# Performance work log

Measured on AMD Instinct MI355X. Metric: run time of the kernel, lower is better.

The kernel has to match this reference:

```python
import jax, jax.numpy as jnp
import numpy as np

IN_FEATURES = 1024
OUT_FEATURES = 1024
BATCH = 32768
EPS = 1e-6


def setup_inputs() -> dict:
    key = jax.random.key(0)
    kx, kw = jax.random.split(key)
    x = jax.random.normal(kx, (BATCH, IN_FEATURES), dtype=jnp.float32)
    # xavier-uniform-like init for weight [out, in]
    limit = np.sqrt(6.0 / (IN_FEATURES + OUT_FEATURES)).astype(np.float32)
    W = jax.random.uniform(kw, (OUT_FEATURES, IN_FEATURES), dtype=jnp.float32,
                           minval=-limit, maxval=limit)
    b = jnp.zeros((OUT_FEATURES,), dtype=jnp.float32)
    return {"x": x, "W": W, "b": b}


def reference(x, W, b):
    # sign with sign(0) -> +1
    binary_w = jnp.where(W >= 0, 1.0, -1.0).astype(W.dtype)  # [out, in]
    # per-output-row scale, detached in the original (no grad flows through it)
    scale = jnp.maximum(jnp.mean(jnp.abs(W), axis=1, keepdims=True), EPS)  # [out, 1]
    # F.linear(x, binary_w * scale, b) = x @ (binary_w * scale).T + b
    return jnp.einsum('ni,oi->no', x, binary_w * scale) + b
```

## Files before the change

### kernel.cpp

```cpp
#include <hip/hip_runtime.h>


typedef short short8 __attribute__((ext_vector_type(8)));
typedef float f32x4 __attribute__((ext_vector_type(4)));

#define BATCH 32768
#define IN_F  1024
#define OUT_F 1024
#define EPS   1e-6f

__device__ __forceinline__ ushort f2bf(float f) {
  unsigned u = __builtin_bit_cast(unsigned, f);
  u += 0x7FFFu + ((u >> 16) & 1u);
  return (ushort)(u >> 16);
}

__device__ __forceinline__ void gload_lds16(const void* g, void* l) {
  __builtin_amdgcn_global_load_lds(
      (const __attribute__((address_space(1))) unsigned*)g,
      (__attribute__((address_space(3))) unsigned*)l, 16, 0, 0);
}

__global__ void bin_kernel(const float* __restrict__ W,
                           ushort* __restrict__ Wb,
                           float* __restrict__ scale) {
  int row = blockIdx.x * 4 + (threadIdx.x >> 6);
  int t = threadIdx.x & 63;
  const float4* wr = (const float4*)(W + (size_t)row * IN_F);
  ushort4* wb = (ushort4*)(Wb + (size_t)row * IN_F);
  float s = 0.f;
#pragma unroll
  for (int i = 0; i < 4; ++i) {
    float4 v = wr[i * 64 + t];
    ushort4 u;
    u.x = (v.x >= 0.f) ? 0x3F80 : 0xBF80;
    u.y = (v.y >= 0.f) ? 0x3F80 : 0xBF80;
    u.z = (v.z >= 0.f) ? 0x3F80 : 0xBF80;
    u.w = (v.w >= 0.f) ? 0x3F80 : 0xBF80;
    wb[i * 64 + t] = u;
    s += fabsf(v.x) + fabsf(v.y) + fabsf(v.z) + fabsf(v.w);
  }
#pragma unroll
  for (int o = 32; o > 0; o >>= 1) s += __shfl_down(s, o);
  if (t == 0) scale[row] = fmaxf(s * (1.0f / (float)IN_F), EPS);
}

__global__ void cvt_kernel(const float* __restrict__ X,
                           ushort* __restrict__ Xb) {
  size_t idx = (size_t)blockIdx.x * 256 + threadIdx.x;
  float4 v = ((const float4*)X)[idx];
  ushort4 u;
  u.x = f2bf(v.x); u.y = f2bf(v.y); u.z = f2bf(v.z); u.w = f2bf(v.w);
  ((ushort4*)Xb)[idx] = u;
}

__device__ __forceinline__ void rd4(short8 (*dst)[2], const char* base,
                                    int c0, int c1) {
#pragma unroll
  for (int m = 0; m < 4; ++m) {
    dst[m][0] = *(const short8*)(base + m * 2048 + c0);
    dst[m][1] = *(const short8*)(base + m * 2048 + c1);
  }
}
__device__ __forceinline__ void rd2(short8 (*dst)[2], const char* base,
                                    int c0, int c1) {
#pragma unroll
  for (int n = 0; n < 2; ++n) {
    dst[n][0] = *(const short8*)(base + n * 2048 + c0);
    dst[n][1] = *(const short8*)(base + n * 2048 + c1);
  }
}
template <int MB, int NB>
__device__ __forceinline__ void mmq(f32x4 (*acc)[4], const short8 (*a)[2],
                                    const short8 (*b)[2]) {
#pragma unroll
  for (int ks = 0; ks < 2; ++ks)
#pragma unroll
    for (int m = 0; m < 4; ++m)
#pragma unroll
      for (int n = 0; n < 2; ++n)
        acc[MB + m][NB + n] = __builtin_amdgcn_mfma_f32_16x16x32_bf16(
            a[m][ks], b[n][ks], acc[MB + m][NB + n], 0, 0, 0);
}

#define FENCE() do { __builtin_amdgcn_sched_barrier(0); \
                     asm volatile("" ::: "memory"); } while (0)
#define BAR()   do { FENCE(); __builtin_amdgcn_s_barrier(); FENCE(); } while (0)
#define MFMA_SEC(stmt) do { BAR(); __builtin_amdgcn_s_setprio(1); stmt; \
                            __builtin_amdgcn_s_setprio(0); BAR(); } while (0)

__global__ __launch_bounds__(512, 2) void gemm8p(
    const ushort* __restrict__ Xb, const ushort* __restrict__ Wb,
    const float* __restrict__ scale, const float* __restrict__ bias,
    float* __restrict__ out) {
  __shared__ __align__(16) char L[131072];

  int bid = blockIdx.x;
  int g = (bid & 7) * 64 + (bid >> 3);
  int mt = g >> 2, nt = g & 3;
  int rowBase = mt * 256, colBase = nt * 256;

  int tid = threadIdx.x, lane = tid & 63, w = tid >> 6;
  int wm = w >> 2, wn = w & 3;

  int baseA = (wm * 128 + (lane & 15)) * 128;
  int baseB = 65536 + (wn * 64 + (lane & 15)) * 128;
  int c0 = ((lane >> 4) * 16) ^ ((lane & 7) << 4);
  int c1 = c0 ^ 64;
  int srl = lane >> 3;
  int scb = ((lane & 7) ^ srl) * 8;
  int bu0 = (w & 3) * 8 + (w >> 2) * 64;
  const ushort* gA = Xb + ((size_t)rowBase + srl) * IN_F + scb;
  const ushort* gB = Wb + ((size_t)colBase + srl) * IN_F + scb;

#define STA(bufOff, kt, row0) \
  gload_lds16(gA + (size_t)(row0) * IN_F + (kt) * 64, L + (bufOff) + (row0) * 128)
#define STB(bufOff, kt, row0) \
  gload_lds16(gB + (size_t)(row0) * IN_F + (kt) * 64, \
              L + 65536 + (bufOff) + (row0) * 128)

  f32x4 acc[8][4];
#pragma unroll
  for (int m = 0; m < 8; ++m)
#pragma unroll
    for (int n = 0; n < 4; ++n) acc[m][n] = (f32x4){0.f, 0.f, 0.f, 0.f};

  STA(0, 0, w * 8);        STA(0, 0, 128 + w * 8);
  STA(0, 0, 64 + w * 8);   STA(0, 0, 192 + w * 8);
  STB(0, 0, bu0);          STB(0, 0, bu0 + 128);
  STB(0, 0, bu0 + 32);     STB(0, 0, bu0 + 160);
  STA(32768, 1, w * 8);      STA(32768, 1, 128 + w * 8);
  STA(32768, 1, 64 + w * 8); STA(32768, 1, 192 + w * 8);
  STB(32768, 1, bu0);        STB(32768, 1, bu0 + 128);
  STB(32768, 1, bu0 + 32);   STB(32768, 1, bu0 + 160);
  asm volatile("s_waitcnt vmcnt(8)");
  BAR();

  short8 aLo[4][2], aHi[4][2], bb[2][2];

  for (int it = 0; it < 8; ++it) {
    int kt2 = (2 * it + 2) & 15;
    int kt3 = (2 * it + 3) & 15;

    rd4(aLo, L + baseA, c0, c1);
    rd2(bb, L + baseB, c0, c1);
    MFMA_SEC((mmq<0, 0>(acc, aLo, bb)));
    rd4(aHi, L + baseA + 4 * 2048, c0, c1);
    STA(0, kt2, w * 8); STA(0, kt2, 128 + w * 8);
    MFMA_SEC((mmq<4, 0>(acc, aHi, bb)));
    rd2(bb, L + baseB + 2 * 2048, c0, c1);
    STB(0, kt2, bu0); STB(0, kt2, bu0 + 128);
    MFMA_SEC((mmq<4, 2>(acc, aHi, bb)));
    STA(0, kt2, 64 + w * 8); STA(0, kt2, 192 + w * 8);
    asm volatile("s_waitcnt vmcnt(6)");
    MFMA_SEC((mmq<0, 2>(acc, aLo, bb)));

    rd4(aLo, L + 32768 + baseA, c0, c1);
    rd2(bb, L + 32768 + baseB, c0, c1);
    STB(0, kt2, bu0 + 32); STB(0, kt2, bu0 + 160);
    MFMA_SEC((mmq<0, 0>(acc, aLo, bb)));
    rd4(aHi, L + 32768 + baseA + 4 * 2048, c0, c1);
    STA(32768, kt3, w * 8); STA(32768, kt3, 128 + w * 8);
    MFMA_SEC((mmq<4, 0>(acc, aHi, bb)));
    rd2(bb, L + 32768 + baseB + 2 * 2048, c0, c1);
    STB(32768, kt3, bu0); STB(32768, kt3, bu0 + 128);
    MFMA_SEC((mmq<4, 2>(acc, aHi, bb)));
    STA(32768, kt3, 64 + w * 8); STA(32768, kt3, 192 + w * 8);
    STB(32768, kt3, bu0 + 32);   STB(32768, kt3, bu0 + 160);
    asm volatile("s_waitcnt vmcnt(6)");
    MFMA_SEC((mmq<0, 2>(acc, aLo, bb)));
  }

  asm volatile("s_waitcnt vmcnt(0)");

#pragma unroll
  for (int n = 0; n < 4; ++n) {
    int col = colBase + wn * 64 + n * 16 + (lane & 15);
    float sc = scale[col];
    float bs = bias[col];
#pragma unroll
    for (int m = 0; m < 8; ++m) {
      int r0 = rowBase + wm * 128 + m * 16 + ((lane >> 4) << 2);
#pragma unroll
      for (int j = 0; j < 4; ++j)
        out[(size_t)(r0 + j) * OUT_F + col] = acc[m][n][j] * sc + bs;
    }
  }
#undef STA
#undef STB
}

__global__ void gemm_kernel(const float* __restrict__ X,
                            const ushort* __restrict__ Wb,
                            const float* __restrict__ scale,
                            const float* __restrict__ bias,
                            float* __restrict__ out) {
  __shared__ __align__(16) ushort lA[128 * 32];
  __shared__ __align__(16) ushort lB[128 * 32];
  int bid = blockIdx.x;
  int g = (bid & 7) * 256 + (bid >> 3);
  int mt = g >> 3, nt = g & 7;
  int rowBase = mt * 128, colBase = nt * 128;
  int t = threadIdx.x, lane = t & 63, wave = t >> 6;
  int wr = wave >> 1, wc = wave & 1;
  f32x4 acc[4][4];
#pragma unroll
  for (int m = 0; m < 4; ++m)
#pragma unroll
    for (int n = 0; n < 4; ++n) acc[m][n] = (f32x4){0.f, 0.f, 0.f, 0.f};
  for (int kk = 0; kk < IN_F / 32; ++kk) {
    int k0 = kk * 32;
    __syncthreads();
#pragma unroll
    for (int i = 0; i < 2; ++i) {
      int idx = t + 256 * i;
      int r = idx >> 2, c16 = idx & 3;
      const float4* gp =
          (const float4*)(X + (size_t)(rowBase + r) * IN_F + k0 + c16 * 8);
      float4 v0 = gp[0];
      float4 v1 = gp[1];
      short8 u;
      u[0] = (short)f2bf(v0.x); u[1] = (short)f2bf(v0.y);
      u[2] = (short)f2bf(v0.z); u[3] = (short)f2bf(v0.w);
      u[4] = (short)f2bf(v1.x); u[5] = (short)f2bf(v1.y);
      u[6] = (short)f2bf(v1.z); u[7] = (short)f2bf(v1.w);
      int off = (r * 32 + c16 * 8) ^ ((r & 7) << 3);
      *(short8*)(&lA[off]) = u;
      const short8* gp2 =
          (const short8*)(Wb + (size_t)(colBase + r) * IN_F + k0 + c16 * 8);
      *(short8*)(&lB[off]) = *gp2;
    }
    __syncthreads();
    short8 af[4], bfr[4];
#pragma unroll
    for (int m = 0; m < 4; ++m) {
      int r = wr * 64 + m * 16 + (lane & 15);
      int off = (r * 32 + (lane >> 4) * 8) ^ ((r & 7) << 3);
      af[m] = *(const short8*)(&lA[off]);
    }
#pragma unroll
    for (int n = 0; n < 4; ++n) {
      int r = wc * 64 + n * 16 + (lane & 15);
      int off = (r * 32 + (lane >> 4) * 8) ^ ((r & 7) << 3);
      bfr[n] = *(const short8*)(&lB[off]);
    }
#pragma unroll
    for (int m = 0; m < 4; ++m)
#pragma unroll
      for (int n = 0; n < 4; ++n)
        acc[m][n] = __builtin_amdgcn_mfma_f32_16x16x32_bf16(
            af[m], bfr[n], acc[m][n], 0, 0, 0);
  }
#pragma unroll
  for (int n = 0; n < 4; ++n) {
    int col = colBase + wc * 64 + n * 16 + (lane & 15);
    float sc = scale[col];
    float bs = bias[col];
#pragma unroll
    for (int m = 0; m < 4; ++m) {
      int r0 = rowBase + wr * 64 + m * 16 + ((lane >> 4) << 2);
#pragma unroll
      for (int j = 0; j < 4; ++j)
        out[(size_t)(r0 + j) * OUT_F + col] = acc[m][n][j] * sc + bs;
    }
  }
}

extern "C" void kernel_launch(void* const* d_in, const int* in_sizes, int n_in,
                              void* d_out, int out_size, void* d_ws,
                              size_t ws_size, hipStream_t stream) {
  const float* x = (const float*)d_in[0];
  const float* W = (const float*)d_in[1];
  const float* b = (const float*)d_in[2];
  float* out = (float*)d_out;

  float* scale = (float*)d_ws;
  ushort* Wb = (ushort*)((char*)d_ws + 4096);
  ushort* xb = (ushort*)((char*)d_ws + 4096 + 2097152);
  const size_t need = 4096 + 2097152 + (size_t)BATCH * IN_F * 2;

  bin_kernel<<<OUT_F / 4, 256, 0, stream>>>(W, Wb, scale);

  if (ws_size >= need) {
    cvt_kernel<<<(BATCH * IN_F / 4) / 256, 256, 0, stream>>>(x, xb);
    gemm8p<<<(BATCH / 256) * (OUT_F / 256), 512, 0, stream>>>(xb, Wb, scale,
                                                              b, out);
  } else {
    gemm_kernel<<<(BATCH / 128) * (OUT_F / 128), 256, 0, stream>>>(
        x, Wb, scale, b, out);
  }
}
```

Measured before the change: 298.3 us.

## Fuse fp32-to-bf16 conversion of X into the GEMM A-tile loading

Removes the separate cvt_kernel pass that wrote a bf16 copy of X. The GEMM now loads fp32 X through registers, converts it to bf16 in-kernel and writes it to LDS, in place of the direct global-to-LDS loads. This saves a full read and write of X plus one kernel launch. The cost is extra VGPR pressure, VALU conversion work and a register round-trip inside the MFMA pipeline. Each K-tile of A also reads twice as many bytes, since the fp32 source is loaded four times per tile (128MB total over the 4 N-tiles).

```diff
diff --git a/kernel.cpp b/kernel.cpp
--- a/kernel.cpp
+++ b/kernel.cpp
@@ -45,15 +45,6 @@
   if (t == 0) scale[row] = fmaxf(s * (1.0f / (float)IN_F), EPS);
 }
 
-__global__ void cvt_kernel(const float* __restrict__ X,
-                           ushort* __restrict__ Xb) {
-  size_t idx = (size_t)blockIdx.x * 256 + threadIdx.x;
-  float4 v = ((const float4*)X)[idx];
-  ushort4 u;
-  u.x = f2bf(v.x); u.y = f2bf(v.y); u.z = f2bf(v.z); u.w = f2bf(v.w);
-  ((ushort4*)Xb)[idx] = u;
-}
-
 __device__ __forceinline__ void rd4(short8 (*dst)[2], const char* base,
                                     int c0, int c1) {
 #pragma unroll
@@ -89,8 +80,8 @@
 #define MFMA_SEC(stmt) do { BAR(); __builtin_amdgcn_s_setprio(1); stmt; \
                             __builtin_amdgcn_s_setprio(0); BAR(); } while (0)
 
-__global__ __launch_bounds__(512, 2) void gemm8p(
-    const ushort* __restrict__ Xb, const ushort* __restrict__ Wb,
+__global__ __launch_bounds__(512, 2) void gemm8pf(
+    const float* __restrict__ X, const ushort* __restrict__ Wb,
     const float* __restrict__ scale, const float* __restrict__ bias,
     float* __restrict__ out) {
   __shared__ __align__(16) char L[131072];
@@ -110,11 +101,20 @@
   int srl = lane >> 3;
   int scb = ((lane & 7) ^ srl) * 8;
   int bu0 = (w & 3) * 8 + (w >> 2) * 64;
-  const ushort* gA = Xb + ((size_t)rowBase + srl) * IN_F + scb;
-  const ushort* gB = Wb + ((size_t)colBase + srl) * IN_F + scb;
-
-#define STA(bufOff, kt, row0) \
-  gload_lds16(gA + (size_t)(row0) * IN_F + (kt) * 64, L + (bufOff) + (row0) * 128)
+  const float*  gAf = X  + ((size_t)rowBase + srl) * IN_F + scb;
+  const ushort* gB  = Wb + ((size_t)colBase + srl) * IN_F + scb;
+
+#define ALOAD(v0, v1, v2, v3, kt, r0a, r0b) do { \
+    const float* p0 = gAf + (size_t)(r0a) * IN_F + (kt) * 64; \
+    const float* p1 = gAf + (size_t)(r0b) * IN_F + (kt) * 64; \
+    v0 = *(const float4*)p0; v1 = *(const float4*)(p0 + 4); \
+    v2 = *(const float4*)p1; v3 = *(const float4*)(p1 + 4); } while (0)
+#define CVTW1(v0, v1, dstOff) do { short8 u; \
+    u[0] = (short)f2bf(v0.x); u[1] = (short)f2bf(v0.y); \
+    u[2] = (short)f2bf(v0.z); u[3] = (short)f2bf(v0.w); \
+    u[4] = (short)f2bf(v1.x); u[5] = (short)f2bf(v1.y); \
+    u[6] = (short)f2bf(v1.z); u[7] = (short)f2bf(v1.w); \
+    *(short8*)(L + (dstOff) + lane * 16) = u; } while (0)
 #define STB(bufOff, kt, row0) \
   gload_lds16(gB + (size_t)(row0) * IN_F + (kt) * 64, \
               L + 65536 + (bufOff) + (row0) * 128)
@@ -125,15 +125,28 @@
 #pragma unroll
     for (int n = 0; n < 4; ++n) acc[m][n] = (f32x4){0.f, 0.f, 0.f, 0.f};
 
-  STA(0, 0, w * 8);        STA(0, 0, 128 + w * 8);
-  STA(0, 0, 64 + w * 8);   STA(0, 0, 192 + w * 8);
-  STB(0, 0, bu0);          STB(0, 0, bu0 + 128);
-  STB(0, 0, bu0 + 32);     STB(0, 0, bu0 + 160);
-  STA(32768, 1, w * 8);      STA(32768, 1, 128 + w * 8);
-  STA(32768, 1, 64 + w * 8); STA(32768, 1, 192 + w * 8);
-  STB(32768, 1, bu0);        STB(32768, 1, bu0 + 128);
-  STB(32768, 1, bu0 + 32);   STB(32768, 1, bu0 + 160);
-  asm volatile("s_waitcnt vmcnt(8)");
+  float4 xa0, xa1, xa2, xa3;
+  float4 xb0, xb1, xb2, xb3;
+  float4 pa0, pa1, pa2, pa3, pb0, pb1, pb2, pb3;
+
+  ALOAD(pa0, pa1, pa2, pa3, 0, w * 8, 128 + w * 8);
+  ALOAD(pb0, pb1, pb2, pb3, 0, 64 + w * 8, 192 + w * 8);
+  STB(0, 0, bu0); STB(0, 0, bu0 + 128);
+  STB(0, 0, bu0 + 32); STB(0, 0, bu0 + 160);
+  ALOAD(xa0, xa1, xa2, xa3, 1, w * 8, 128 + w * 8);
+  ALOAD(xb0, xb1, xb2, xb3, 1, 64 + w * 8, 192 + w * 8);
+  STB(32768, 1, bu0); STB(32768, 1, bu0 + 128);
+  STB(32768, 1, bu0 + 32); STB(32768, 1, bu0 + 160);
+  CVTW1(pa0, pa1, (w * 8) * 128);
+  CVTW1(pa2, pa3, (128 + w * 8) * 128);
+  CVTW1(pb0, pb1, (64 + w * 8) * 128);
+  CVTW1(pb2, pb3, (192 + w * 8) * 128);
+  CVTW1(xa0, xa1, 32768 + (w * 8) * 128);
+  CVTW1(xa2, xa3, 32768 + (128 + w * 8) * 128);
+  CVTW1(xb0, xb1, 32768 + (64 + w * 8) * 128);
+  CVTW1(xb2, xb3, 32768 + (192 + w * 8) * 128);
+  asm volatile("s_waitcnt lgkmcnt(0)" ::: "memory");
+  asm volatile("s_waitcnt vmcnt(4)");
   BAR();
 
   short8 aLo[4][2], aHi[4][2], bb[2][2];
@@ -144,29 +157,39 @@
 
     rd4(aLo, L + baseA, c0, c1);
     rd2(bb, L + baseB, c0, c1);
+    ALOAD(xa0, xa1, xa2, xa3, kt2, w * 8, 128 + w * 8);
     MFMA_SEC((mmq<0, 0>(acc, aLo, bb)));
-    rd4(aHi, L + baseA + 4 * 2048, c0, c1);
-    STA(0, kt2, w * 8); STA(0, kt2, 128 + w * 8);
+    CVTW1(xa0, xa1, (w * 8) * 128);
+    CVTW1(xa2, xa3, (128 + w * 8) * 128);
+    rd4(aHi, L + baseA + 8192, c0, c1);
     MFMA_SEC((mmq<4, 0>(acc, aHi, bb)));
-    rd2(bb, L + baseB + 2 * 2048, c0, c1);
+    ALOAD(xb0, xb1, xb2, xb3, kt2, 64 + w * 8, 192 + w * 8);
     STB(0, kt2, bu0); STB(0, kt2, bu0 + 128);
+    rd2(bb, L + baseB + 4096, c0, c1);
     MFMA_SEC((mmq<4, 2>(acc, aHi, bb)));
-    STA(0, kt2, 64 + w * 8); STA(0, kt2, 192 + w * 8);
+    CVTW1(xb0, xb1, (64 + w * 8) * 128);
+    CVTW1(xb2, xb3, (192 + w * 8) * 128);
+    asm volatile("s_waitcnt lgkmcnt(0)" ::: "memory");
     asm volatile("s_waitcnt vmcnt(6)");
     MFMA_SEC((mmq<0, 2>(acc, aLo, bb)));
 
     rd4(aLo, L + 32768 + baseA, c0, c1);
     rd2(bb, L + 32768 + baseB, c0, c1);
+    ALOAD(xa0, xa1, xa2, xa3, kt3, w * 8, 128 + w * 8);
     STB(0, kt2, bu0 + 32); STB(0, kt2, bu0 + 160);
     MFMA_SEC((mmq<0, 0>(acc, aLo, bb)));
-    rd4(aHi, L + 32768 + baseA + 4 * 2048, c0, c1);
-    STA(32768, kt3, w * 8); STA(32768, kt3, 128 + w * 8);
+    CVTW1(xa0, xa1, 32768 + (w * 8) * 128);
+    CVTW1(xa2, xa3, 32768 + (128 + w * 8) * 128);
+    rd4(aHi, L + 32768 + baseA + 8192, c0, c1);
     MFMA_SEC((mmq<4, 0>(acc, aHi, bb)));
-    rd2(bb, L + 32768 + baseB + 2 * 2048, c0, c1);
+    ALOAD(xb0, xb1, xb2, xb3, kt3, 64 + w * 8, 192 + w * 8);
     STB(32768, kt3, bu0); STB(32768, kt3, bu0 + 128);
+    rd2(bb, L + 32768 + baseB + 4096, c0, c1);
     MFMA_SEC((mmq<4, 2>(acc, aHi, bb)));
-    STA(32768, kt3, 64 + w * 8); STA(32768, kt3, 192 + w * 8);
-    STB(32768, kt3, bu0 + 32);   STB(32768, kt3, bu0 + 160);
+    CVTW1(xb0, xb1, 32768 + (64 + w * 8) * 128);
+    CVTW1(xb2, xb3, 32768 + (192 + w * 8) * 128);
+    STB(32768, kt3, bu0 + 32); STB(32768, kt3, bu0 + 160);
+    asm volatile("s_waitcnt lgkmcnt(0)" ::: "memory");
     asm volatile("s_waitcnt vmcnt(6)");
     MFMA_SEC((mmq<0, 2>(acc, aLo, bb)));
   }
@@ -186,7 +209,8 @@
         out[(size_t)(r0 + j) * OUT_F + col] = acc[m][n][j] * sc + bs;
     }
   }
-#undef STA
+#undef ALOAD
+#undef CVTW1
 #undef STB
 }
 
@@ -276,15 +300,13 @@
 
   float* scale = (float*)d_ws;
   ushort* Wb = (ushort*)((char*)d_ws + 4096);
-  ushort* xb = (ushort*)((char*)d_ws + 4096 + 2097152);
-  const size_t need = 4096 + 2097152 + (size_t)BATCH * IN_F * 2;
+  const size_t need = 4096 + 2097152;
 
   bin_kernel<<<OUT_F / 4, 256, 0, stream>>>(W, Wb, scale);
 
   if (ws_size >= need) {
-    cvt_kernel<<<(BATCH * IN_F / 4) / 256, 256, 0, stream>>>(x, xb);
-    gemm8p<<<(BATCH / 256) * (OUT_F / 256), 512, 0, stream>>>(xb, Wb, scale,
-                                                              b, out);
+    gemm8pf<<<(BATCH / 256) * (OUT_F / 256), 512, 0, stream>>>(x, Wb, scale,
+                                                               b, out);
   } else {
     gemm_kernel<<<(BATCH / 128) * (OUT_F / 128), 256, 0, stream>>>(
         x, Wb, scale, b, out);
```

After: 338.9 us. +13.6%, slower.
